# Optimization experiments

Measured on AMD Instinct MI355X. Metric: run time of the kernel, lower is better.

The kernel has to match this reference:

```python
import jax, jax.numpy as jnp
import numpy as np

EMBED = 1024
HEADS = 16
HEAD_DIM = EMBED // HEADS
SCALE = HEAD_DIM ** -0.5


def setup_inputs() -> dict:
    key = jax.random.key(0)
    ks = jax.random.split(key, 9)
    B, N = 2, 2048
    std = EMBED ** -0.5
    return {
        "query": jax.random.normal(ks[0], (B, N, EMBED), jnp.float32),
        "key": jax.random.normal(ks[1], (B, N, EMBED), jnp.float32),
        "value": jax.random.normal(ks[2], (B, N, EMBED), jnp.float32),
        # torch nn.Linear weights are [out, in]; y = x @ W.T + b
        "Wq": jax.random.normal(ks[3], (EMBED, EMBED), jnp.float32) * std,
        "bq": jax.random.normal(ks[4], (EMBED,), jnp.float32) * 0.01,
        "Wk": jax.random.normal(ks[5], (EMBED, EMBED), jnp.float32) * std,
        "bk": jax.random.normal(ks[6], (EMBED,), jnp.float32) * 0.01,
        "Wv": jax.random.normal(ks[7], (EMBED, EMBED), jnp.float32) * std,
        "bv": jax.random.normal(ks[8], (EMBED,), jnp.float32) * 0.01,
    }


def reference(query, key, value, Wq, bq, Wk, bk, Wv, bv):
    B, NQ, _ = query.shape
    NK = key.shape[1]
    q = query @ Wq.T + bq  # [B, NQ, E]
    k = key @ Wk.T + bk    # [B, NK, E]
    v = value @ Wv.T + bv  # [B, NK, E]
    # split heads -> [B, H, N, Dh]
    q = q.reshape(B, NQ, HEADS, HEAD_DIM).transpose(0, 2, 1, 3)
    k = k.reshape(B, NK, HEADS, HEAD_DIM).transpose(0, 2, 1, 3)
    v = v.reshape(B, NK, HEADS, HEAD_DIM).transpose(0, 2, 1, 3)
    attn = jnp.einsum("bhqd,bhkd->bhqk", q, k) * SCALE  # [B, H, NQ, NK]
    attn = jax.nn.softmax(attn, axis=-1)
    out = jnp.einsum("bhqk,bhkd->bhqd", attn, v)  # [B, H, NQ, Dh]
    out = out.transpose(0, 2, 1, 3).reshape(B, NQ, EMBED)
    # o_proj is Identity (odim == embed_dim, o_proj=False); dropout is 0 (eval)
    return out
```

## Files before the change

### kernel.cpp

```cpp
#include <hip/hip_runtime.h>

#define EMB 1024
#define NSEQ 2048
#define NBATCH 2
#define NHEAD 16
#define DHEAD 64
#define QSCALE 0.18033688011112042f

typedef float f32x4 __attribute__((ext_vector_type(4)));
typedef short s16x8 __attribute__((ext_vector_type(8)));
typedef short s16x4 __attribute__((ext_vector_type(4)));

typedef __attribute__((address_space(3))) short lds_short;
typedef __attribute__((address_space(1))) const short glb_short;

__device__ __forceinline__ void gl_lds16(const short* g, short* l) {
    __builtin_amdgcn_global_load_lds((glb_short*)g, (lds_short*)l, 16, 0, 0);
}

__device__ __forceinline__ short bf16r(float f) {
    unsigned u = __float_as_uint(f);
    u += 0x7fffu + ((u >> 16) & 1u);
    return (short)(u >> 16);
}

__device__ __forceinline__ unsigned pkbf(float a, float b) {
#if defined(__has_builtin) && __has_builtin(__builtin_amdgcn_cvt_pk_bf16_f32)
    auto r = __builtin_amdgcn_cvt_pk_bf16_f32(a, b);
    unsigned u;
    __builtin_memcpy(&u, &r, 4);
    return u;
#else
    return ((unsigned)bf16r(a) & 0xffffu) | ((unsigned)bf16r(b) << 16);
#endif
}

__device__ __forceinline__ float fexp2(float x) {
#if defined(__has_builtin) && __has_builtin(__builtin_amdgcn_exp2f)
    return __builtin_amdgcn_exp2f(x);
#else
    return exp2f(x);
#endif
}

__global__ __launch_bounds__(256) void cvt6_kernel(
    const float* __restrict__ s0, const float* __restrict__ s1, const float* __restrict__ s2,
    const float* __restrict__ s3, const float* __restrict__ s4, const float* __restrict__ s5,
    short* __restrict__ d0, short* __restrict__ d1, short* __restrict__ d2,
    short* __restrict__ d3, short* __restrict__ d4, short* __restrict__ d5,
    int n0, int n1, int n2, int n3, int n4, int n5)
{
    const int seg = blockIdx.y;
    const float* s = (seg == 0) ? s0 : (seg == 1) ? s1 : (seg == 2) ? s2
                   : (seg == 3) ? s3 : (seg == 4) ? s4 : s5;
    short* d = (seg == 0) ? d0 : (seg == 1) ? d1 : (seg == 2) ? d2
             : (seg == 3) ? d3 : (seg == 4) ? d4 : d5;
    const int n = (seg == 0) ? n0 : (seg == 1) ? n1 : (seg == 2) ? n2
                : (seg == 3) ? n3 : (seg == 4) ? n4 : n5;

    const int i = (blockIdx.x * 256 + threadIdx.x) * 8;
    if (i >= n) return;
    float4 a = *(const float4*)(s + i);
    float4 b = *(const float4*)(s + i + 4);
    uint4 u = { pkbf(a.x, a.y), pkbf(a.z, a.w), pkbf(b.x, b.y), pkbf(b.z, b.w) };
    *(uint4*)(d + i) = u;
}

__global__ __launch_bounds__(256) void proj2_kernel(
    const short* __restrict__ Xq, const short* __restrict__ Xk, const short* __restrict__ Xv,
    const short* __restrict__ Wq, const short* __restrict__ Wk, const short* __restrict__ Wv,
    const float* __restrict__ bq, const float* __restrict__ bk, const float* __restrict__ bv,
    short* __restrict__ Oq, short* __restrict__ Ok, short* __restrict__ Ov)
{
    const int z = blockIdx.z;
    const short* X    = (z == 0) ? Xq : (z == 1) ? Xk : Xv;
    const short* W    = (z == 0) ? Wq : (z == 1) ? Wk : Wv;
    const float* bias = (z == 0) ? bq : (z == 1) ? bk : bv;
    short* Out        = (z == 0) ? Oq : (z == 1) ? Ok : Ov;
    const float osc   = (z == 0) ? QSCALE : 1.0f;

    const int n0 = blockIdx.x * 128;
    const int m0 = blockIdx.y * 128;

    __shared__ __align__(16) short As[128 * 32];
    __shared__ __align__(16) short Bs[128 * 32];

    const int t    = threadIdx.x;
    const int lane = t & 63;
    const int wave = t >> 6;
    const int r    = lane & 15;
    const int quad = lane >> 4;
    const int wm   = (wave >> 1) * 64;
    const int wn   = (wave & 1) * 64;

    const int flat0 = t * 16;
    const int flat1 = flat0 + 4096;
    const int row0  = flat0 >> 6;
    const int row1  = flat1 >> 6;
    const int cs0   = (((flat0 >> 4) & 3) ^ (row0 & 3)) * 8;
    const int cs1   = (((flat1 >> 4) & 3) ^ (row1 & 3)) * 8;

    const short* ga0 = X + (size_t)(m0 + row0) * EMB + cs0;
    const short* ga1 = X + (size_t)(m0 + row1) * EMB + cs1;
    const short* gb0 = W + (size_t)(n0 + row0) * EMB + cs0;
    const short* gb1 = W + (size_t)(n0 + row1) * EMB + cs1;
    short* la0 = As + (flat0 >> 1);
    short* la1 = As + (flat1 >> 1);
    short* lb0 = Bs + (flat0 >> 1);
    short* lb1 = Bs + (flat1 >> 1);

    f32x4 acc[4][4];
#pragma unroll
    for (int i = 0; i < 4; ++i)
#pragma unroll
        for (int j = 0; j < 4; ++j)
#pragma unroll
            for (int v = 0; v < 4; ++v) acc[i][j][v] = 0.f;

    const int fcol = (quad ^ (r & 3)) * 8;

    for (int k0 = 0; k0 < EMB; k0 += 32) {
        gl_lds16(ga0 + k0, la0);
        gl_lds16(ga1 + k0, la1);
        gl_lds16(gb0 + k0, lb0);
        gl_lds16(gb1 + k0, lb1);
        __syncthreads();

        s16x8 af[4], bf[4];
#pragma unroll
        for (int i = 0; i < 4; ++i) af[i] = *(const s16x8*)&As[(wm + i * 16 + r) * 32 + fcol];
#pragma unroll
        for (int j = 0; j < 4; ++j) bf[j] = *(const s16x8*)&Bs[(wn + j * 16 + r) * 32 + fcol];
#pragma unroll
        for (int i = 0; i < 4; ++i)
#pragma unroll
            for (int j = 0; j < 4; ++j)
                acc[i][j] = __builtin_amdgcn_mfma_f32_16x16x32_bf16(af[i], bf[j], acc[i][j], 0, 0, 0);
        __syncthreads();
    }

#pragma unroll
    for (int j = 0; j < 4; ++j) {
        const int gn = n0 + wn + j * 16 + r;
        const float bb = bias[gn];
#pragma unroll
        for (int i = 0; i < 4; ++i)
#pragma unroll
            for (int reg = 0; reg < 4; ++reg) {
                const int gm = m0 + wm + i * 16 + quad * 4 + reg;
                Out[(size_t)gm * EMB + gn] = bf16r((acc[i][j][reg] + bb) * osc);
            }
    }
}

__global__ __launch_bounds__(256) void proj_kernel(
    const float* __restrict__ Xq, const float* __restrict__ Xk, const float* __restrict__ Xv,
    const float* __restrict__ Wq, const float* __restrict__ Wk, const float* __restrict__ Wv,
    const float* __restrict__ bq, const float* __restrict__ bk, const float* __restrict__ bv,
    short* __restrict__ Oq, short* __restrict__ Ok, short* __restrict__ Ov)
{
    const int z = blockIdx.z;
    const float* X    = (z == 0) ? Xq : (z == 1) ? Xk : Xv;
    const float* W    = (z == 0) ? Wq : (z == 1) ? Wk : Wv;
    const float* bias = (z == 0) ? bq : (z == 1) ? bk : bv;
    short* Out        = (z == 0) ? Oq : (z == 1) ? Ok : Ov;
    const float osc   = (z == 0) ? QSCALE : 1.0f;

    const int n0 = blockIdx.x * 128;
    const int m0 = blockIdx.y * 128;

    __shared__ __align__(16) short As[128][40];
    __shared__ __align__(16) short Bs[128][40];

    const int t    = threadIdx.x;
    const int lane = t & 63;
    const int wave = t >> 6;
    const int r    = lane & 15;
    const int quad = lane >> 4;
    const int wm   = (wave >> 1) * 64;
    const int wn   = (wave & 1) * 64;

    const int srow = t >> 1;
    const int scol = (t & 1) << 4;

    f32x4 acc[4][4];
#pragma unroll
    for (int i = 0; i < 4; ++i)
#pragma unroll
        for (int j = 0; j < 4; ++j)
#pragma unroll
            for (int v = 0; v < 4; ++v) acc[i][j][v] = 0.f;

    for (int k0 = 0; k0 < EMB; k0 += 32) {
        const float4* xp = (const float4*)(X + (size_t)(m0 + srow) * EMB + k0 + scol);
        const float4* wp = (const float4*)(W + (size_t)(n0 + srow) * EMB + k0 + scol);
        float4 x0 = xp[0], x1 = xp[1], x2 = xp[2], x3 = xp[3];
        float4 w0 = wp[0], w1 = wp[1], w2 = wp[2], w3 = wp[3];
        uint4 a0 = { pkbf(x0.x, x0.y), pkbf(x0.z, x0.w), pkbf(x1.x, x1.y), pkbf(x1.z, x1.w) };
        uint4 a1 = { pkbf(x2.x, x2.y), pkbf(x2.z, x2.w), pkbf(x3.x, x3.y), pkbf(x3.z, x3.w) };
        uint4 b0 = { pkbf(w0.x, w0.y), pkbf(w0.z, w0.w), pkbf(w1.x, w1.y), pkbf(w1.z, w1.w) };
        uint4 b1 = { pkbf(w2.x, w2.y), pkbf(w2.z, w2.w), pkbf(w3.x, w3.y), pkbf(w3.z, w3.w) };
        *(uint4*)&As[srow][scol]     = a0;
        *(uint4*)&As[srow][scol + 8] = a1;
        *(uint4*)&Bs[srow][scol]     = b0;
        *(uint4*)&Bs[srow][scol + 8] = b1;
        __syncthreads();

        s16x8 af[4], bf[4];
#pragma unroll
        for (int i = 0; i < 4; ++i) af[i] = *(const s16x8*)&As[wm + i * 16 + r][quad * 8];
#pragma unroll
        for (int j = 0; j < 4; ++j) bf[j] = *(const s16x8*)&Bs[wn + j * 16 + r][quad * 8];
#pragma unroll
        for (int i = 0; i < 4; ++i)
#pragma unroll
            for (int j = 0; j < 4; ++j)
                acc[i][j] = __builtin_amdgcn_mfma_f32_16x16x32_bf16(af[i], bf[j], acc[i][j], 0, 0, 0);
        __syncthreads();
    }

#pragma unroll
    for (int j = 0; j < 4; ++j) {
        const int gn = n0 + wn + j * 16 + r;
        const float bb = bias[gn];
#pragma unroll
        for (int i = 0; i < 4; ++i)
#pragma unroll
            for (int reg = 0; reg < 4; ++reg) {
                const int gm = m0 + wm + i * 16 + quad * 4 + reg;
                Out[(size_t)gm * EMB + gn] = bf16r((acc[i][j][reg] + bb) * osc);
            }
    }
}

__global__ __launch_bounds__(256) void vtrans_kernel(
    const short* __restrict__ Vp, short* __restrict__ VT)
{
    const int n0 = blockIdx.x * 64;
    const int h  = blockIdx.y;
    const int b  = blockIdx.z;
    __shared__ __align__(16) short L[64][72];

    const int t  = threadIdx.x;
    const int rr = t >> 2;
    const int cc = (t & 3) * 16;

    const short* src = Vp + (size_t)(b * NSEQ + n0 + rr) * EMB + h * DHEAD + cc;
    s16x8 a = *(const s16x8*)src;
    s16x8 c = *(const s16x8*)(src + 8);
    *(s16x8*)&L[rr][cc]     = a;
    *(s16x8*)&L[rr][cc + 8] = c;
    __syncthreads();

    const int d  = t >> 2;
    const int c4 = (t & 3) * 16;
    short vals[16];
#pragma unroll
    for (int i = 0; i < 16; ++i) vals[i] = L[c4 + i][d];
    short* dst = VT + ((size_t)(b * NHEAD + h) * DHEAD + d) * NSEQ + n0 + c4;
    *(s16x8*)dst       = *(s16x8*)&vals[0];
    *(s16x8*)(dst + 8) = *(s16x8*)&vals[8];
}

__global__ __launch_bounds__(256, 2) void attn2_kernel(
    const short* __restrict__ Qp, const short* __restrict__ Kp,
    const short* __restrict__ VT, float* __restrict__ Out)
{
    const int qblk = blockIdx.x * 128;
    const int h    = blockIdx.y;
    const int b    = blockIdx.z;

    __shared__ __align__(16) short Ks[64][72];
    __shared__ __align__(16) short Vs[64][72];
    __shared__ __align__(16) float fbuf[4][16][68];

    const int t    = threadIdx.x;
    const int lane = t & 63;
    const int w    = t >> 6;
    const int r    = lane & 15;
    const int quad = lane >> 4;

    const size_t rowbase = (size_t)b * NSEQ;
    const int colbase    = h * DHEAD;

    s16x8 qf[2][2];
#pragma unroll
    for (int qs = 0; qs < 2; ++qs)
#pragma unroll
        for (int ks = 0; ks < 2; ++ks)
            qf[qs][ks] = *(const s16x8*)(Qp + (rowbase + qblk + w * 32 + qs * 16 + r) * EMB
                                          + colbase + ks * 32 + quad * 8);

    f32x4 accO[2][4];
    float lsum[2] = {0.f, 0.f};
#pragma unroll
    for (int qs = 0; qs < 2; ++qs)
#pragma unroll
        for (int dt = 0; dt < 4; ++dt)
#pragma unroll
            for (int v = 0; v < 4; ++v) accO[qs][dt][v] = 0.f;

    const int srow = t >> 2;
    const int scol = (t & 3) << 4;

    const short* Kbase = Kp + (rowbase + srow) * EMB + colbase + scol;
    const short* Vbase = VT + ((size_t)(b * NHEAD + h) * DHEAD + srow) * NSEQ + scol;

    for (int kt = 0; kt < 32; ++kt) {
        const short* Ksrc = Kbase + (size_t)(kt * 64) * EMB;
        const short* Vsrc = Vbase + kt * 64;
        s16x8 k0 = *(const s16x8*)Ksrc, k1 = *(const s16x8*)(Ksrc + 8);
        s16x8 v0 = *(const s16x8*)Vsrc, v1 = *(const s16x8*)(Vsrc + 8);
        *(s16x8*)&Ks[srow][scol]     = k0;
        *(s16x8*)&Ks[srow][scol + 8] = k1;
        *(s16x8*)&Vs[srow][scol]     = v0;
        *(s16x8*)&Vs[srow][scol + 8] = v1;
        __syncthreads();

        s16x8 kf[4][2];
#pragma unroll
        for (int jt = 0; jt < 4; ++jt)
#pragma unroll
            for (int ks = 0; ks < 2; ++ks)
                kf[jt][ks] = *(const s16x8*)&Ks[jt * 16 + r][ks * 32 + quad * 8];

        s16x8 vf[4][2];
#pragma unroll
        for (int dt = 0; dt < 4; ++dt)
#pragma unroll
            for (int s = 0; s < 2; ++s) {
                s16x4 lo = *(const s16x4*)&Vs[dt * 16 + r][s * 32 + quad * 4];
                s16x4 hi = *(const s16x4*)&Vs[dt * 16 + r][s * 32 + 16 + quad * 4];
                vf[dt][s] = __builtin_shufflevector(lo, hi, 0, 1, 2, 3, 4, 5, 6, 7);
            }

        s16x8 pf[2][2];
#pragma unroll
        for (int qs = 0; qs < 2; ++qs) {
            f32x4 sacc[4];
#pragma unroll
            for (int jt = 0; jt < 4; ++jt) {
#pragma unroll
                for (int v = 0; v < 4; ++v) sacc[jt][v] = 0.f;
#pragma unroll
                for (int ks = 0; ks < 2; ++ks)
                    sacc[jt] = __builtin_amdgcn_mfma_f32_16x16x32_bf16(kf[jt][ks], qf[qs][ks], sacc[jt], 0, 0, 0);
            }
            float p[4][4];
#pragma unroll
            for (int jt = 0; jt < 4; ++jt)
#pragma unroll
                for (int reg = 0; reg < 4; ++reg) {
                    p[jt][reg] = fexp2(sacc[jt][reg]);
                    lsum[qs] += p[jt][reg];
                }
#pragma unroll
            for (int s = 0; s < 2; ++s) {
                uint4 uu = { pkbf(p[2 * s][0],     p[2 * s][1]),
                             pkbf(p[2 * s][2],     p[2 * s][3]),
                             pkbf(p[2 * s + 1][0], p[2 * s + 1][1]),
                             pkbf(p[2 * s + 1][2], p[2 * s + 1][3]) };
                __builtin_memcpy(&pf[qs][s], &uu, 16);
            }
        }

#pragma unroll
        for (int qs = 0; qs < 2; ++qs)
#pragma unroll
            for (int dt = 0; dt < 4; ++dt) {
                accO[qs][dt] = __builtin_amdgcn_mfma_f32_16x16x32_bf16(vf[dt][0], pf[qs][0], accO[qs][dt], 0, 0, 0);
                accO[qs][dt] = __builtin_amdgcn_mfma_f32_16x16x32_bf16(vf[dt][1], pf[qs][1], accO[qs][dt], 0, 0, 0);
            }
        __syncthreads();
    }

    float rl[2];
#pragma unroll
    for (int qs = 0; qs < 2; ++qs) {
        float s = lsum[qs];
        s += __shfl_xor(s, 16);
        s += __shfl_xor(s, 32);
        rl[qs] = 1.f / s;
    }

#pragma unroll
    for (int qs = 0; qs < 2; ++qs) {
        __syncthreads();
#pragma unroll
        for (int dt = 0; dt < 4; ++dt)
#pragma unroll
            for (int reg = 0; reg < 4; ++reg)
                fbuf[w][r][dt * 16 + quad * 4 + reg] = accO[qs][dt][reg] * rl[qs];
        __syncthreads();
        const int qi   = t >> 2;
        const int c    = (t & 3) * 16;
        const int wsrc = qi >> 4;
        const int rsrc = qi & 15;
        const float4* fp = (const float4*)&fbuf[wsrc][rsrc][c];
        float4 o0 = fp[0], o1 = fp[1], o2 = fp[2], o3 = fp[3];
        float* op = Out + (rowbase + qblk + wsrc * 32 + qs * 16 + rsrc) * EMB + colbase + c;
        ((float4*)op)[0] = o0;
        ((float4*)op)[1] = o1;
        ((float4*)op)[2] = o2;
        ((float4*)op)[3] = o3;
    }
}

__global__ __launch_bounds__(256) void attn_fb_kernel(
    const short* __restrict__ Qp, const short* __restrict__ Kp,
    const short* __restrict__ Vp, float* __restrict__ Out)
{
    const int qt = blockIdx.x;
    const int h  = blockIdx.y;
    const int b  = blockIdx.z;

    __shared__ __align__(16) short Ks[64][72];
    __shared__ __align__(16) short VsT[64][72];
    __shared__ __align__(16) short Ps[4][16][72];

    const int t    = threadIdx.x;
    const int lane = t & 63;
    const int w    = t >> 6;
    const int r    = lane & 15;
    const int quad = lane >> 4;

    const size_t rowbase = (size_t)b * NSEQ;
    const int colbase    = h * DHEAD;

    const short* Qr = Qp + (rowbase + qt * 64 + w * 16 + r) * EMB + colbase;
    const s16x8 qf0 = *(const s16x8*)(Qr + quad * 8);
    const s16x8 qf1 = *(const s16x8*)(Qr + 32 + quad * 8);

    float mrow[4], lrow[4];
    f32x4 accO[4];
#pragma unroll
    for (int i = 0; i < 4; ++i) {
        mrow[i] = -INFINITY;
        lrow[i] = 0.f;
#pragma unroll
        for (int v = 0; v < 4; ++v) accO[i][v] = 0.f;
    }

    const int srow = t >> 2;
    const int scol = (t & 3) << 4;

    for (int kt = 0; kt < 32; ++kt) {
        const short* Krow = Kp + (rowbase + kt * 64 + srow) * EMB + colbase + scol;
        const short* Vrow = Vp + (rowbase + kt * 64 + srow) * EMB + colbase + scol;
        s16x8 kv0 = *(const s16x8*)Krow;
        s16x8 kv1 = *(const s16x8*)(Krow + 8);
        s16x8 vv0 = *(const s16x8*)Vrow;
        s16x8 vv1 = *(const s16x8*)(Vrow + 8);
        *(s16x8*)&Ks[srow][scol]     = kv0;
        *(s16x8*)&Ks[srow][scol + 8] = kv1;
#pragma unroll
        for (int i = 0; i < 8; ++i) {
            VsT[scol + i][srow]     = vv0[i];
            VsT[scol + 8 + i][srow] = vv1[i];
        }
        __syncthreads();

        f32x4 sacc[4];
#pragma unroll
        for (int j = 0; j < 4; ++j) {
#pragma unroll
            for (int v = 0; v < 4; ++v) sacc[j][v] = 0.f;
            s16x8 kf0 = *(const s16x8*)&Ks[j * 16 + r][quad * 8];
            s16x8 kf1 = *(const s16x8*)&Ks[j * 16 + r][32 + quad * 8];
            sacc[j] = __builtin_amdgcn_mfma_f32_16x16x32_bf16(qf0, kf0, sacc[j], 0, 0, 0);
            sacc[j] = __builtin_amdgcn_mfma_f32_16x16x32_bf16(qf1, kf1, sacc[j], 0, 0, 0);
        }

        float rmax[4];
#pragma unroll
        for (int reg = 0; reg < 4; ++reg) rmax[reg] = -INFINITY;
#pragma unroll
        for (int j = 0; j < 4; ++j)
#pragma unroll
            for (int reg = 0; reg < 4; ++reg)
                rmax[reg] = fmaxf(rmax[reg], sacc[j][reg]);
#pragma unroll
        for (int reg = 0; reg < 4; ++reg) {
#pragma unroll
            for (int mask = 1; mask <= 8; mask <<= 1)
                rmax[reg] = fmaxf(rmax[reg], __shfl_xor(rmax[reg], mask, 64));
        }

        float alpha[4], rsum[4];
#pragma unroll
        for (int reg = 0; reg < 4; ++reg) {
            float mnew = fmaxf(mrow[reg], rmax[reg]);
            alpha[reg] = fexp2(mrow[reg] - mnew);
            mrow[reg]  = mnew;
            rsum[reg]  = 0.f;
        }

#pragma unroll
        for (int j = 0; j < 4; ++j)
#pragma unroll
            for (int reg = 0; reg < 4; ++reg) {
                float p = fexp2(sacc[j][reg] - mrow[reg]);
                rsum[reg] += p;
                Ps[w][quad * 4 + reg][j * 16 + r] = bf16r(p);
            }
#pragma unroll
        for (int reg = 0; reg < 4; ++reg) {
#pragma unroll
            for (int mask = 1; mask <= 8; mask <<= 1)
                rsum[reg] += __shfl_xor(rsum[reg], mask, 64);
            lrow[reg] = lrow[reg] * alpha[reg] + rsum[reg];
        }
#pragma unroll
        for (int j = 0; j < 4; ++j)
#pragma unroll
            for (int reg = 0; reg < 4; ++reg) accO[j][reg] *= alpha[reg];

#pragma unroll
        for (int s = 0; s < 2; ++s) {
            s16x8 pfr = *(const s16x8*)&Ps[w][r][s * 32 + quad * 8];
#pragma unroll
            for (int j = 0; j < 4; ++j) {
                s16x8 vfr = *(const s16x8*)&VsT[j * 16 + r][s * 32 + quad * 8];
                accO[j] = __builtin_amdgcn_mfma_f32_16x16x32_bf16(pfr, vfr, accO[j], 0, 0, 0);
            }
        }
        __syncthreads();
    }

#pragma unroll
    for (int j = 0; j < 4; ++j)
#pragma unroll
        for (int reg = 0; reg < 4; ++reg) {
            const int qrow = qt * 64 + w * 16 + quad * 4 + reg;
            Out[(rowbase + qrow) * EMB + colbase + j * 16 + r] = accO[j][reg] / lrow[reg];
        }
}

extern "C" void kernel_launch(void* const* d_in, const int* in_sizes, int n_in,
                              void* d_out, int out_size, void* d_ws, size_t ws_size,
                              hipStream_t stream) {
    const float* query = (const float*)d_in[0];
    const float* key   = (const float*)d_in[1];
    const float* value = (const float*)d_in[2];
    const float* Wq    = (const float*)d_in[3];
    const float* bq    = (const float*)d_in[4];
    const float* Wk    = (const float*)d_in[5];
    const float* bk    = (const float*)d_in[6];
    const float* Wv    = (const float*)d_in[7];
    const float* bv    = (const float*)d_in[8];
    float* out = (float*)d_out;

    const size_t XBUF = (size_t)NBATCH * NSEQ * EMB;
    const size_t WBUF = (size_t)EMB * EMB;

    short* Qb  = (short*)d_ws;
    short* Kb  = Qb + XBUF;
    short* Vb  = Kb + XBUF;
    short* VTb = Vb + XBUF;
    short* Xqb = VTb + XBUF;
    short* Xkb = Xqb + XBUF;
    short* Xvb = Xkb + XBUF;
    short* Wqb = Xvb + XBUF;
    short* Wkb = Wqb + WBUF;
    short* Wvb = Wkb + WBUF;

    const size_t need_full  = (7 * XBUF + 3 * WBUF) * sizeof(short);
    const size_t need_attn2 = 4 * XBUF * sizeof(short);

    if (ws_size >= need_full) {
        cvt6_kernel<<<dim3(2048, 6), 256, 0, stream>>>(
            query, key, value, Wq, Wk, Wv,
            Xqb, Xkb, Xvb, Wqb, Wkb, Wvb,
            (int)XBUF, (int)XBUF, (int)XBUF, (int)WBUF, (int)WBUF, (int)WBUF);
        proj2_kernel<<<dim3(EMB / 128, (NBATCH * NSEQ) / 128, 3), 256, 0, stream>>>(
            Xqb, Xkb, Xvb, Wqb, Wkb, Wvb, bq, bk, bv, Qb, Kb, Vb);
        vtrans_kernel<<<dim3(NSEQ / 64, NHEAD, NBATCH), 256, 0, stream>>>(Vb, VTb);
        attn2_kernel<<<dim3(NSEQ / 128, NHEAD, NBATCH), 256, 0, stream>>>(Qb, Kb, VTb, out);
    } else if (ws_size >= need_attn2) {
        proj_kernel<<<dim3(EMB / 128, (NBATCH * NSEQ) / 128, 3), 256, 0, stream>>>(
            query, key, value, Wq, Wk, Wv, bq, bk, bv, Qb, Kb, Vb);
        vtrans_kernel<<<dim3(NSEQ / 64, NHEAD, NBATCH), 256, 0, stream>>>(Vb, VTb);
        attn2_kernel<<<dim3(NSEQ / 128, NHEAD, NBATCH), 256, 0, stream>>>(Qb, Kb, VTb, out);
    } else {
        proj_kernel<<<dim3(EMB / 128, (NBATCH * NSEQ) / 128, 3), 256, 0, stream>>>(
            query, key, value, Wq, Wk, Wv, bq, bk, bv, Qb, Kb, Vb);
        attn_fb_kernel<<<dim3(NSEQ / 64, NHEAD, NBATCH), 256, 0, stream>>>(Qb, Kb, Vb, out);
    }
}
```

Baseline: 207.2 us.

## Split attention keys across waves and widen projection K-tile

The attention kernel now gives each block 64 queries and splits each 128-key tile across the four waves, so every wave handles 32 keys for all 64 queries. The waves' partial outputs and row sums are combined through shared memory at the end. K/V tiles are staged with direct global-to-LDS loads into XOR-swizzled layouts. The projection GEMM doubles its K-step to 64 with a wider swizzle and asks for three blocks per SM; this halves the barrier count but adds a cross-wave reduction and more LDS per block.

New measurement: 241.6 us. 1.17x slower.

```diff
diff --git a/kernel.cpp b/kernel.cpp
--- a/kernel.cpp
+++ b/kernel.cpp
@@ -66,7 +66,7 @@
     *(uint4*)(d + i) = u;
 }
 
-__global__ __launch_bounds__(256) void proj2_kernel(
+__global__ __launch_bounds__(256, 3) void proj2_kernel(
     const short* __restrict__ Xq, const short* __restrict__ Xk, const short* __restrict__ Xv,
     const short* __restrict__ Wq, const short* __restrict__ Wk, const short* __restrict__ Wv,
     const float* __restrict__ bq, const float* __restrict__ bk, const float* __restrict__ bv,
@@ -82,8 +82,8 @@
     const int n0 = blockIdx.x * 128;
     const int m0 = blockIdx.y * 128;
 
-    __shared__ __align__(16) short As[128 * 32];
-    __shared__ __align__(16) short Bs[128 * 32];
+    __shared__ __align__(16) short As[128 * 64];
+    __shared__ __align__(16) short Bs[128 * 64];
 
     const int t    = threadIdx.x;
     const int lane = t & 63;
@@ -93,21 +93,13 @@
     const int wm   = (wave >> 1) * 64;
     const int wn   = (wave & 1) * 64;
 
-    const int flat0 = t * 16;
-    const int flat1 = flat0 + 4096;
-    const int row0  = flat0 >> 6;
-    const int row1  = flat1 >> 6;
-    const int cs0   = (((flat0 >> 4) & 3) ^ (row0 & 3)) * 8;
-    const int cs1   = (((flat1 >> 4) & 3) ^ (row1 & 3)) * 8;
-
-    const short* ga0 = X + (size_t)(m0 + row0) * EMB + cs0;
-    const short* ga1 = X + (size_t)(m0 + row1) * EMB + cs1;
-    const short* gb0 = W + (size_t)(n0 + row0) * EMB + cs0;
-    const short* gb1 = W + (size_t)(n0 + row1) * EMB + cs1;
-    short* la0 = As + (flat0 >> 1);
-    short* la1 = As + (flat1 >> 1);
-    short* lb0 = Bs + (flat0 >> 1);
-    short* lb1 = Bs + (flat1 >> 1);
+    const int p0    = wave * 256 + lane;
+    const int row0  = p0 >> 3;
+    const int lc0   = (p0 & 7) ^ (row0 & 7);
+    const short* gA = X + (size_t)(m0 + row0) * EMB + lc0 * 8;
+    const short* gB = W + (size_t)(n0 + row0) * EMB + lc0 * 8;
+    short* lA = As + p0 * 8;
+    short* lB = Bs + p0 * 8;
 
     f32x4 acc[4][4];
 #pragma unroll
@@ -117,25 +109,28 @@
 #pragma unroll
             for (int v = 0; v < 4; ++v) acc[i][j][v] = 0.f;
 
-    const int fcol = (quad ^ (r & 3)) * 8;
-
-    for (int k0 = 0; k0 < EMB; k0 += 32) {
-        gl_lds16(ga0 + k0, la0);
-        gl_lds16(ga1 + k0, la1);
-        gl_lds16(gb0 + k0, lb0);
-        gl_lds16(gb1 + k0, lb1);
-        __syncthreads();
-
-        s16x8 af[4], bf[4];
-#pragma unroll
-        for (int i = 0; i < 4; ++i) af[i] = *(const s16x8*)&As[(wm + i * 16 + r) * 32 + fcol];
-#pragma unroll
-        for (int j = 0; j < 4; ++j) bf[j] = *(const s16x8*)&Bs[(wn + j * 16 + r) * 32 + fcol];
-#pragma unroll
-        for (int i = 0; i < 4; ++i)
-#pragma unroll
-            for (int j = 0; j < 4; ++j)
-                acc[i][j] = __builtin_amdgcn_mfma_f32_16x16x32_bf16(af[i], bf[j], acc[i][j], 0, 0, 0);
+    for (int k0 = 0; k0 < EMB; k0 += 64) {
+#pragma unroll
+        for (int i = 0; i < 4; ++i) {
+            gl_lds16(gA + k0 + (size_t)8 * i * EMB, lA + i * 512);
+            gl_lds16(gB + k0 + (size_t)8 * i * EMB, lB + i * 512);
+        }
+        __syncthreads();
+
+#pragma unroll
+        for (int ks = 0; ks < 2; ++ks) {
+            const int fc = ((ks * 4 + quad) ^ (r & 7)) * 8;
+            s16x8 af[4], bf[4];
+#pragma unroll
+            for (int i = 0; i < 4; ++i) af[i] = *(const s16x8*)&As[(wm + i * 16 + r) * 64 + fc];
+#pragma unroll
+            for (int j = 0; j < 4; ++j) bf[j] = *(const s16x8*)&Bs[(wn + j * 16 + r) * 64 + fc];
+#pragma unroll
+            for (int i = 0; i < 4; ++i)
+#pragma unroll
+                for (int j = 0; j < 4; ++j)
+                    acc[i][j] = __builtin_amdgcn_mfma_f32_16x16x32_bf16(af[i], bf[j], acc[i][j], 0, 0, 0);
+        }
         __syncthreads();
     }
 
@@ -262,17 +257,20 @@
     *(s16x8*)(dst + 8) = *(s16x8*)&vals[8];
 }
 
-__global__ __launch_bounds__(256, 2) void attn2_kernel(
+__global__ __launch_bounds__(256, 3) void attn3_kernel(
     const short* __restrict__ Qp, const short* __restrict__ Kp,
     const short* __restrict__ VT, float* __restrict__ Out)
 {
-    const int qblk = blockIdx.x * 128;
+    const int qblk = blockIdx.x * 64;
     const int h    = blockIdx.y;
     const int b    = blockIdx.z;
 
-    __shared__ __align__(16) short Ks[64][72];
-    __shared__ __align__(16) short Vs[64][72];
-    __shared__ __align__(16) float fbuf[4][16][68];
+    __shared__ __align__(16) char smem[35840];
+    short* KsS  = (short*)smem;
+    short* VsS  = (short*)smem + 128 * 64;
+    float* bufA = (float*)smem;
+    float* bufB = (float*)smem + 64 * 68;
+    float* l4   = (float*)smem + 2 * 64 * 68;
 
     const int t    = threadIdx.x;
     const int lane = t & 63;
@@ -281,128 +279,149 @@
     const int quad = lane >> 4;
 
     const size_t rowbase = (size_t)b * NSEQ;
-    const int colbase    = h * DHEAD;
-
-    s16x8 qf[2][2];
-#pragma unroll
-    for (int qs = 0; qs < 2; ++qs)
+    const int    colbase = h * DHEAD;
+    const size_t bh64    = (size_t)(b * NHEAD + h) * DHEAD;
+
+    s16x8 qf[4][2];
+#pragma unroll
+    for (int qt = 0; qt < 4; ++qt)
 #pragma unroll
         for (int ks = 0; ks < 2; ++ks)
-            qf[qs][ks] = *(const s16x8*)(Qp + (rowbase + qblk + w * 32 + qs * 16 + r) * EMB
+            qf[qt][ks] = *(const s16x8*)(Qp + (rowbase + qblk + qt * 16 + r) * EMB
                                           + colbase + ks * 32 + quad * 8);
 
-    f32x4 accO[2][4];
-    float lsum[2] = {0.f, 0.f};
-#pragma unroll
-    for (int qs = 0; qs < 2; ++qs)
+    const int pk0   = w * 256 + lane;
+    const int krow0 = pk0 >> 3;
+    const int klc   = (pk0 & 7) ^ (krow0 & 7);
+    const short* gK = Kp + (rowbase + krow0) * EMB + colbase + klc * 8;
+    short* lK = KsS + pk0 * 8;
+
+    const short* gV[4];
+    short* lV[4];
+#pragma unroll
+    for (int i = 0; i < 4; ++i) {
+        const int p   = (w * 4 + i) * 64 + lane;
+        const int row = p >> 4;
+        const int lc  = (p & 15) ^ (row & 15);
+        gV[i] = VT + (bh64 + row) * NSEQ + lc * 8;
+        lV[i] = VsS + p * 8;
+    }
+
+    f32x4 accO[4][4];
+    float lsum[4] = {0.f, 0.f, 0.f, 0.f};
+#pragma unroll
+    for (int qt = 0; qt < 4; ++qt)
 #pragma unroll
         for (int dt = 0; dt < 4; ++dt)
 #pragma unroll
-            for (int v = 0; v < 4; ++v) accO[qs][dt][v] = 0.f;
-
-    const int srow = t >> 2;
-    const int scol = (t & 3) << 4;
-
-    const short* Kbase = Kp + (rowbase + srow) * EMB + colbase + scol;
-    const short* Vbase = VT + ((size_t)(b * NHEAD + h) * DHEAD + srow) * NSEQ + scol;
-
-    for (int kt = 0; kt < 32; ++kt) {
-        const short* Ksrc = Kbase + (size_t)(kt * 64) * EMB;
-        const short* Vsrc = Vbase + kt * 64;
-        s16x8 k0 = *(const s16x8*)Ksrc, k1 = *(const s16x8*)(Ksrc + 8);
-        s16x8 v0 = *(const s16x8*)Vsrc, v1 = *(const s16x8*)(Vsrc + 8);
-        *(s16x8*)&Ks[srow][scol]     = k0;
-        *(s16x8*)&Ks[srow][scol + 8] = k1;
-        *(s16x8*)&Vs[srow][scol]     = v0;
-        *(s16x8*)&Vs[srow][scol + 8] = v1;
-        __syncthreads();
-
-        s16x8 kf[4][2];
-#pragma unroll
-        for (int jt = 0; jt < 4; ++jt)
+            for (int v = 0; v < 4; ++v) accO[qt][dt][v] = 0.f;
+
+    for (int kt = 0; kt < 16; ++kt) {
+#pragma unroll
+        for (int i = 0; i < 4; ++i) {
+            gl_lds16(gK + (size_t)(kt * 128 + 8 * i) * EMB, lK + i * 512);
+            gl_lds16(gV[i] + kt * 128, lV[i]);
+        }
+        __syncthreads();
+
+        s16x8 kf[2][2];
+#pragma unroll
+        for (int jt = 0; jt < 2; ++jt)
 #pragma unroll
             for (int ks = 0; ks < 2; ++ks)
-                kf[jt][ks] = *(const s16x8*)&Ks[jt * 16 + r][ks * 32 + quad * 8];
-
-        s16x8 vf[4][2];
-#pragma unroll
-        for (int dt = 0; dt < 4; ++dt)
-#pragma unroll
-            for (int s = 0; s < 2; ++s) {
-                s16x4 lo = *(const s16x4*)&Vs[dt * 16 + r][s * 32 + quad * 4];
-                s16x4 hi = *(const s16x4*)&Vs[dt * 16 + r][s * 32 + 16 + quad * 4];
-                vf[dt][s] = __builtin_shufflevector(lo, hi, 0, 1, 2, 3, 4, 5, 6, 7);
+                kf[jt][ks] = *(const s16x8*)&KsS[(w * 32 + jt * 16 + r) * 64
+                                                 + (((ks * 4 + quad) ^ (r & 7)) * 8)];
+
+        s16x8 vfx[4];
+#pragma unroll
+        for (int dt = 0; dt < 4; ++dt) {
+            const int ph0 = (4 * w + (quad >> 1)) ^ r;
+            const int ph1 = (4 * w + 2 + (quad >> 1)) ^ r;
+            s16x4 lo = *(const s16x4*)&VsS[(dt * 16 + r) * 128 + ph0 * 8 + (quad & 1) * 4];
+            s16x4 hi = *(const s16x4*)&VsS[(dt * 16 + r) * 128 + ph1 * 8 + (quad & 1) * 4];
+            vfx[dt] = __builtin_shufflevector(lo, hi, 0, 1, 2, 3, 4, 5, 6, 7);
+        }
+
+#pragma unroll
+        for (int qt = 0; qt < 4; ++qt) {
+            f32x4 sacc[2];
+#pragma unroll
+            for (int jt = 0; jt < 2; ++jt) {
+#pragma unroll
+                for (int v = 0; v < 4; ++v) sacc[jt][v] = 0.f;
+#pragma unroll
+                for (int ks = 0; ks < 2; ++ks)
+                    sacc[jt] = __builtin_amdgcn_mfma_f32_16x16x32_bf16(kf[jt][ks], qf[qt][ks], sacc[jt], 0, 0, 0);
             }
-
-        s16x8 pf[2][2];
-#pragma unroll
-        for (int qs = 0; qs < 2; ++qs) {
-            f32x4 sacc[4];
-#pragma unroll
-            for (int jt = 0; jt < 4; ++jt) {
-#pragma unroll
-                for (int v = 0; v < 4; ++v) sacc[jt][v] = 0.f;
-#pragma unroll
-                for (int ks = 0; ks < 2; ++ks)
-                    sacc[jt] = __builtin_amdgcn_mfma_f32_16x16x32_bf16(kf[jt][ks], qf[qs][ks], sacc[jt], 0, 0, 0);
-            }
-            float p[4][4];
-#pragma unroll
-            for (int jt = 0; jt < 4; ++jt)
+            float p[2][4];
+#pragma unroll
+            for (int jt = 0; jt < 2; ++jt)
 #pragma unroll
                 for (int reg = 0; reg < 4; ++reg) {
                     p[jt][reg] = fexp2(sacc[jt][reg]);
-                    lsum[qs] += p[jt][reg];
+                    lsum[qt] += p[jt][reg];
                 }
-#pragma unroll
-            for (int s = 0; s < 2; ++s) {
-                uint4 uu = { pkbf(p[2 * s][0],     p[2 * s][1]),
-                             pkbf(p[2 * s][2],     p[2 * s][3]),
-                             pkbf(p[2 * s + 1][0], p[2 * s + 1][1]),
-                             pkbf(p[2 * s + 1][2], p[2 * s + 1][3]) };
-                __builtin_memcpy(&pf[qs][s], &uu, 16);
-            }
-        }
-
-#pragma unroll
-        for (int qs = 0; qs < 2; ++qs)
-#pragma unroll
-            for (int dt = 0; dt < 4; ++dt) {
-                accO[qs][dt] = __builtin_amdgcn_mfma_f32_16x16x32_bf16(vf[dt][0], pf[qs][0], accO[qs][dt], 0, 0, 0);
-                accO[qs][dt] = __builtin_amdgcn_mfma_f32_16x16x32_bf16(vf[dt][1], pf[qs][1], accO[qs][dt], 0, 0, 0);
-            }
-        __syncthreads();
-    }
-
-    float rl[2];
-#pragma unroll
-    for (int qs = 0; qs < 2; ++qs) {
-        float s = lsum[qs];
+            s16x8 pf;
+            uint4 uu = { pkbf(p[0][0], p[0][1]), pkbf(p[0][2], p[0][3]),
+                         pkbf(p[1][0], p[1][1]), pkbf(p[1][2], p[1][3]) };
+            __builtin_memcpy(&pf, &uu, 16);
+#pragma unroll
+            for (int dt = 0; dt < 4; ++dt)
+                accO[qt][dt] = __builtin_amdgcn_mfma_f32_16x16x32_bf16(vfx[dt], pf, accO[qt][dt], 0, 0, 0);
+        }
+        __syncthreads();
+    }
+
+#pragma unroll
+    for (int qt = 0; qt < 4; ++qt) {
+        float s = lsum[qt];
         s += __shfl_xor(s, 16);
         s += __shfl_xor(s, 32);
-        rl[qs] = 1.f / s;
-    }
-
-#pragma unroll
-    for (int qs = 0; qs < 2; ++qs) {
-        __syncthreads();
-#pragma unroll
-        for (int dt = 0; dt < 4; ++dt)
-#pragma unroll
-            for (int reg = 0; reg < 4; ++reg)
-                fbuf[w][r][dt * 16 + quad * 4 + reg] = accO[qs][dt][reg] * rl[qs];
-        __syncthreads();
-        const int qi   = t >> 2;
-        const int c    = (t & 3) * 16;
-        const int wsrc = qi >> 4;
-        const int rsrc = qi & 15;
-        const float4* fp = (const float4*)&fbuf[wsrc][rsrc][c];
-        float4 o0 = fp[0], o1 = fp[1], o2 = fp[2], o3 = fp[3];
-        float* op = Out + (rowbase + qblk + wsrc * 32 + qs * 16 + rsrc) * EMB + colbase + c;
-        ((float4*)op)[0] = o0;
-        ((float4*)op)[1] = o1;
-        ((float4*)op)[2] = o2;
-        ((float4*)op)[3] = o3;
+        if (quad == 0) l4[w * 64 + qt * 16 + r] = s;
+    }
+
+    float* mybuf = (w & 1) ? bufB : bufA;
+    if (w < 2) {
+#pragma unroll
+        for (int qt = 0; qt < 4; ++qt)
+#pragma unroll
+            for (int dt = 0; dt < 4; ++dt)
+                *(f32x4*)&mybuf[(qt * 16 + r) * 68 + dt * 16 + quad * 4] = accO[qt][dt];
+    }
+    __syncthreads();
+    if (w >= 2) {
+#pragma unroll
+        for (int qt = 0; qt < 4; ++qt)
+#pragma unroll
+            for (int dt = 0; dt < 4; ++dt) {
+                f32x4* pp = (f32x4*)&mybuf[(qt * 16 + r) * 68 + dt * 16 + quad * 4];
+                *pp += accO[qt][dt];
+            }
+    }
+    __syncthreads();
+    {
+        const int row = t >> 2;
+        const int c   = (t & 3) * 16;
+#pragma unroll
+        for (int g = 0; g < 4; ++g) {
+            f32x4* pa = (f32x4*)&bufA[row * 68 + c + g * 4];
+            *pa += *(const f32x4*)&bufB[row * 68 + c + g * 4];
+        }
+    }
+    __syncthreads();
+    {
+        const int q = t >> 2;
+        const int c = (t & 3) * 16;
+        const float l  = l4[q] + l4[64 + q] + l4[128 + q] + l4[192 + q];
+        const float rl = 1.f / l;
+        float* op = Out + (rowbase + qblk + q) * EMB + colbase + c;
+#pragma unroll
+        for (int g = 0; g < 4; ++g) {
+            f32x4 o = *(const f32x4*)&bufA[q * 68 + c + g * 4];
+            o *= rl;
+            float4 of = { o[0], o[1], o[2], o[3] };
+            ((float4*)op)[g] = of;
+        }
     }
 }
 
@@ -565,7 +584,7 @@
     short* Wvb = Wkb + WBUF;
 
     const size_t need_full  = (7 * XBUF + 3 * WBUF) * sizeof(short);
-    const size_t need_attn2 = 4 * XBUF * sizeof(short);
+    const size_t need_attn3 = 4 * XBUF * sizeof(short);
 
     if (ws_size >= need_full) {
         cvt6_kernel<<<dim3(2048, 6), 256, 0, stream>>>(
@@ -575,12 +594,12 @@
         proj2_kernel<<<dim3(EMB / 128, (NBATCH * NSEQ) / 128, 3), 256, 0, stream>>>(
             Xqb, Xkb, Xvb, Wqb, Wkb, Wvb, bq, bk, bv, Qb, Kb, Vb);
         vtrans_kernel<<<dim3(NSEQ / 64, NHEAD, NBATCH), 256, 0, stream>>>(Vb, VTb);
-        attn2_kernel<<<dim3(NSEQ / 128, NHEAD, NBATCH), 256, 0, stream>>>(Qb, Kb, VTb, out);
-    } else if (ws_size >= need_attn2) {
+        attn3_kernel<<<dim3(NSEQ / 64, NHEAD, NBATCH), 256, 0, stream>>>(Qb, Kb, VTb, out);
+    } else if (ws_size >= need_attn3) {
         proj_kernel<<<dim3(EMB / 128, (NBATCH * NSEQ) / 128, 3), 256, 0, stream>>>(
             query, key, value, Wq, Wk, Wv, bq, bk, bv, Qb, Kb, Vb);
         vtrans_kernel<<<dim3(NSEQ / 64, NHEAD, NBATCH), 256, 0, stream>>>(Vb, VTb);
-        attn2_kernel<<<dim3(NSEQ / 128, NHEAD, NBATCH), 256, 0, stream>>>(Qb, Kb, VTb, out);
+        attn3_kernel<<<dim3(NSEQ / 64, NHEAD, NBATCH), 256, 0, stream>>>(Qb, Kb, VTb, out);
     } else {
         proj_kernel<<<dim3(EMB / 128, (NBATCH * NSEQ) / 128, 3), 256, 0, stream>>>(
             query, key, value, Wq, Wk, Wv, bq, bk, bv, Qb, Kb, Vb);
```

## Deepen projection GEMM K-tile to 64 and shrink attention query tile to 64

Applied to the files above, without the earlier changes.

The projection GEMM now stages a 64-wide K slice per iteration with an 8-way XOR swizzle. This halves the number of barrier round trips, at the cost of more LDS. The attention kernel drops from 128 to 64 query rows per block (16 per wave) and aliases the output staging buffer onto the K/V shared memory. That cuts register and LDS use so 4 blocks can fit per CU, but it doubles K/V reloads per query row.

After: 221.1 us. 1.07x slower.

```diff
diff --git a/kernel.cpp b/kernel.cpp
--- a/kernel.cpp
+++ b/kernel.cpp
@@ -66,7 +66,7 @@
     *(uint4*)(d + i) = u;
 }
 
-__global__ __launch_bounds__(256) void proj2_kernel(
+__global__ __launch_bounds__(256, 3) void proj2_kernel(
     const short* __restrict__ Xq, const short* __restrict__ Xk, const short* __restrict__ Xv,
     const short* __restrict__ Wq, const short* __restrict__ Wk, const short* __restrict__ Wv,
     const float* __restrict__ bq, const float* __restrict__ bk, const float* __restrict__ bv,
@@ -82,8 +82,8 @@
     const int n0 = blockIdx.x * 128;
     const int m0 = blockIdx.y * 128;
 
-    __shared__ __align__(16) short As[128 * 32];
-    __shared__ __align__(16) short Bs[128 * 32];
+    __shared__ __align__(16) short As[128 * 64];
+    __shared__ __align__(16) short Bs[128 * 64];
 
     const int t    = threadIdx.x;
     const int lane = t & 63;
@@ -93,21 +93,13 @@
     const int wm   = (wave >> 1) * 64;
     const int wn   = (wave & 1) * 64;
 
-    const int flat0 = t * 16;
-    const int flat1 = flat0 + 4096;
-    const int row0  = flat0 >> 6;
-    const int row1  = flat1 >> 6;
-    const int cs0   = (((flat0 >> 4) & 3) ^ (row0 & 3)) * 8;
-    const int cs1   = (((flat1 >> 4) & 3) ^ (row1 & 3)) * 8;
-
-    const short* ga0 = X + (size_t)(m0 + row0) * EMB + cs0;
-    const short* ga1 = X + (size_t)(m0 + row1) * EMB + cs1;
-    const short* gb0 = W + (size_t)(n0 + row0) * EMB + cs0;
-    const short* gb1 = W + (size_t)(n0 + row1) * EMB + cs1;
-    short* la0 = As + (flat0 >> 1);
-    short* la1 = As + (flat1 >> 1);
-    short* lb0 = Bs + (flat0 >> 1);
-    short* lb1 = Bs + (flat1 >> 1);
+    const int p0    = wave * 256 + lane;
+    const int row0  = p0 >> 3;
+    const int lc0   = (p0 & 7) ^ (row0 & 7);
+    const short* gA = X + (size_t)(m0 + row0) * EMB + lc0 * 8;
+    const short* gB = W + (size_t)(n0 + row0) * EMB + lc0 * 8;
+    short* lA = As + p0 * 8;
+    short* lB = Bs + p0 * 8;
 
     f32x4 acc[4][4];
 #pragma unroll
@@ -117,25 +109,28 @@
 #pragma unroll
             for (int v = 0; v < 4; ++v) acc[i][j][v] = 0.f;
 
-    const int fcol = (quad ^ (r & 3)) * 8;
-
-    for (int k0 = 0; k0 < EMB; k0 += 32) {
-        gl_lds16(ga0 + k0, la0);
-        gl_lds16(ga1 + k0, la1);
-        gl_lds16(gb0 + k0, lb0);
-        gl_lds16(gb1 + k0, lb1);
-        __syncthreads();
-
-        s16x8 af[4], bf[4];
-#pragma unroll
-        for (int i = 0; i < 4; ++i) af[i] = *(const s16x8*)&As[(wm + i * 16 + r) * 32 + fcol];
-#pragma unroll
-        for (int j = 0; j < 4; ++j) bf[j] = *(const s16x8*)&Bs[(wn + j * 16 + r) * 32 + fcol];
-#pragma unroll
-        for (int i = 0; i < 4; ++i)
-#pragma unroll
-            for (int j = 0; j < 4; ++j)
-                acc[i][j] = __builtin_amdgcn_mfma_f32_16x16x32_bf16(af[i], bf[j], acc[i][j], 0, 0, 0);
+    for (int k0 = 0; k0 < EMB; k0 += 64) {
+#pragma unroll
+        for (int i = 0; i < 4; ++i) {
+            gl_lds16(gA + k0 + (size_t)8 * i * EMB, lA + i * 512);
+            gl_lds16(gB + k0 + (size_t)8 * i * EMB, lB + i * 512);
+        }
+        __syncthreads();
+
+#pragma unroll
+        for (int ks = 0; ks < 2; ++ks) {
+            const int fc = ((ks * 4 + quad) ^ (r & 7)) * 8;
+            s16x8 af[4], bf[4];
+#pragma unroll
+            for (int i = 0; i < 4; ++i) af[i] = *(const s16x8*)&As[(wm + i * 16 + r) * 64 + fc];
+#pragma unroll
+            for (int j = 0; j < 4; ++j) bf[j] = *(const s16x8*)&Bs[(wn + j * 16 + r) * 64 + fc];
+#pragma unroll
+            for (int i = 0; i < 4; ++i)
+#pragma unroll
+                for (int j = 0; j < 4; ++j)
+                    acc[i][j] = __builtin_amdgcn_mfma_f32_16x16x32_bf16(af[i], bf[j], acc[i][j], 0, 0, 0);
+        }
         __syncthreads();
     }
 
@@ -262,17 +257,18 @@
     *(s16x8*)(dst + 8) = *(s16x8*)&vals[8];
 }
 
-__global__ __launch_bounds__(256, 2) void attn2_kernel(
+__global__ __launch_bounds__(256, 4) void attn5_kernel(
     const short* __restrict__ Qp, const short* __restrict__ Kp,
     const short* __restrict__ VT, float* __restrict__ Out)
 {
-    const int qblk = blockIdx.x * 128;
+    const int qblk = blockIdx.x * 64;
     const int h    = blockIdx.y;
     const int b    = blockIdx.z;
 
-    __shared__ __align__(16) short Ks[64][72];
-    __shared__ __align__(16) short Vs[64][72];
-    __shared__ __align__(16) float fbuf[4][16][68];
+    __shared__ __align__(16) char smem[2 * 64 * 72 * 2];
+    short* Ks   = (short*)smem;
+    short* Vs   = (short*)smem + 64 * 72;
+    float* fbuf = (float*)smem;
 
     const int t    = threadIdx.x;
     const int lane = t & 63;
@@ -281,40 +277,37 @@
     const int quad = lane >> 4;
 
     const size_t rowbase = (size_t)b * NSEQ;
-    const int colbase    = h * DHEAD;
-
-    s16x8 qf[2][2];
-#pragma unroll
-    for (int qs = 0; qs < 2; ++qs)
-#pragma unroll
-        for (int ks = 0; ks < 2; ++ks)
-            qf[qs][ks] = *(const s16x8*)(Qp + (rowbase + qblk + w * 32 + qs * 16 + r) * EMB
-                                          + colbase + ks * 32 + quad * 8);
-
-    f32x4 accO[2][4];
-    float lsum[2] = {0.f, 0.f};
-#pragma unroll
-    for (int qs = 0; qs < 2; ++qs)
-#pragma unroll
-        for (int dt = 0; dt < 4; ++dt)
-#pragma unroll
-            for (int v = 0; v < 4; ++v) accO[qs][dt][v] = 0.f;
+    const int    colbase = h * DHEAD;
+    const size_t bh64    = (size_t)(b * NHEAD + h) * DHEAD;
+
+    s16x8 qf[2];
+#pragma unroll
+    for (int ks = 0; ks < 2; ++ks)
+        qf[ks] = *(const s16x8*)(Qp + (rowbase + qblk + w * 16 + r) * EMB
+                                  + colbase + ks * 32 + quad * 8);
+
+    f32x4 accO[4];
+    float lsum = 0.f;
+#pragma unroll
+    for (int dt = 0; dt < 4; ++dt)
+#pragma unroll
+        for (int v = 0; v < 4; ++v) accO[dt][v] = 0.f;
 
     const int srow = t >> 2;
     const int scol = (t & 3) << 4;
 
     const short* Kbase = Kp + (rowbase + srow) * EMB + colbase + scol;
-    const short* Vbase = VT + ((size_t)(b * NHEAD + h) * DHEAD + srow) * NSEQ + scol;
+    const short* Vbase = VT + (bh64 + srow) * NSEQ + scol;
 
     for (int kt = 0; kt < 32; ++kt) {
         const short* Ksrc = Kbase + (size_t)(kt * 64) * EMB;
         const short* Vsrc = Vbase + kt * 64;
         s16x8 k0 = *(const s16x8*)Ksrc, k1 = *(const s16x8*)(Ksrc + 8);
         s16x8 v0 = *(const s16x8*)Vsrc, v1 = *(const s16x8*)(Vsrc + 8);
-        *(s16x8*)&Ks[srow][scol]     = k0;
-        *(s16x8*)&Ks[srow][scol + 8] = k1;
-        *(s16x8*)&Vs[srow][scol]     = v0;
-        *(s16x8*)&Vs[srow][scol + 8] = v1;
+        *(s16x8*)&Ks[srow * 72 + scol]     = k0;
+        *(s16x8*)&Ks[srow * 72 + scol + 8] = k1;
+        *(s16x8*)&Vs[srow * 72 + scol]     = v0;
+        *(s16x8*)&Vs[srow * 72 + scol + 8] = v1;
         __syncthreads();
 
         s16x8 kf[4][2];
@@ -322,87 +315,75 @@
         for (int jt = 0; jt < 4; ++jt)
 #pragma unroll
             for (int ks = 0; ks < 2; ++ks)
-                kf[jt][ks] = *(const s16x8*)&Ks[jt * 16 + r][ks * 32 + quad * 8];
+                kf[jt][ks] = *(const s16x8*)&Ks[(jt * 16 + r) * 72 + ks * 32 + quad * 8];
 
         s16x8 vf[4][2];
 #pragma unroll
         for (int dt = 0; dt < 4; ++dt)
 #pragma unroll
             for (int s = 0; s < 2; ++s) {
-                s16x4 lo = *(const s16x4*)&Vs[dt * 16 + r][s * 32 + quad * 4];
-                s16x4 hi = *(const s16x4*)&Vs[dt * 16 + r][s * 32 + 16 + quad * 4];
+                s16x4 lo = *(const s16x4*)&Vs[(dt * 16 + r) * 72 + s * 32 + quad * 4];
+                s16x4 hi = *(const s16x4*)&Vs[(dt * 16 + r) * 72 + s * 32 + 16 + quad * 4];
                 vf[dt][s] = __builtin_shufflevector(lo, hi, 0, 1, 2, 3, 4, 5, 6, 7);
             }
 
-        s16x8 pf[2][2];
-#pragma unroll
-        for (int qs = 0; qs < 2; ++qs) {
-            f32x4 sacc[4];
-#pragma unroll
-            for (int jt = 0; jt < 4; ++jt) {
-#pragma unroll
-                for (int v = 0; v < 4; ++v) sacc[jt][v] = 0.f;
-#pragma unroll
-                for (int ks = 0; ks < 2; ++ks)
-                    sacc[jt] = __builtin_amdgcn_mfma_f32_16x16x32_bf16(kf[jt][ks], qf[qs][ks], sacc[jt], 0, 0, 0);
+        f32x4 sacc[4];
+#pragma unroll
+        for (int jt = 0; jt < 4; ++jt) {
+#pragma unroll
+            for (int v = 0; v < 4; ++v) sacc[jt][v] = 0.f;
+#pragma unroll
+            for (int ks = 0; ks < 2; ++ks)
+                sacc[jt] = __builtin_amdgcn_mfma_f32_16x16x32_bf16(kf[jt][ks], qf[ks], sacc[jt], 0, 0, 0);
+        }
+
+        float p[4][4];
+#pragma unroll
+        for (int jt = 0; jt < 4; ++jt)
+#pragma unroll
+            for (int reg = 0; reg < 4; ++reg) {
+                p[jt][reg] = fexp2(sacc[jt][reg]);
+                lsum += p[jt][reg];
             }
-            float p[4][4];
-#pragma unroll
-            for (int jt = 0; jt < 4; ++jt)
-#pragma unroll
-                for (int reg = 0; reg < 4; ++reg) {
-                    p[jt][reg] = fexp2(sacc[jt][reg]);
-                    lsum[qs] += p[jt][reg];
-                }
-#pragma unroll
-            for (int s = 0; s < 2; ++s) {
-                uint4 uu = { pkbf(p[2 * s][0],     p[2 * s][1]),
-                             pkbf(p[2 * s][2],     p[2 * s][3]),
-                             pkbf(p[2 * s + 1][0], p[2 * s + 1][1]),
-                             pkbf(p[2 * s + 1][2], p[2 * s + 1][3]) };
-                __builtin_memcpy(&pf[qs][s], &uu, 16);
-            }
-        }
-
-#pragma unroll
-        for (int qs = 0; qs < 2; ++qs)
-#pragma unroll
-            for (int dt = 0; dt < 4; ++dt) {
-                accO[qs][dt] = __builtin_amdgcn_mfma_f32_16x16x32_bf16(vf[dt][0], pf[qs][0], accO[qs][dt], 0, 0, 0);
-                accO[qs][dt] = __builtin_amdgcn_mfma_f32_16x16x32_bf16(vf[dt][1], pf[qs][1], accO[qs][dt], 0, 0, 0);
-            }
-        __syncthreads();
-    }
-
-    float rl[2];
-#pragma unroll
-    for (int qs = 0; qs < 2; ++qs) {
-        float s = lsum[qs];
-        s += __shfl_xor(s, 16);
-        s += __shfl_xor(s, 32);
-        rl[qs] = 1.f / s;
-    }
-
-#pragma unroll
-    for (int qs = 0; qs < 2; ++qs) {
-        __syncthreads();
-#pragma unroll
-        for (int dt = 0; dt < 4; ++dt)
-#pragma unroll
-            for (int reg = 0; reg < 4; ++reg)
-                fbuf[w][r][dt * 16 + quad * 4 + reg] = accO[qs][dt][reg] * rl[qs];
-        __syncthreads();
-        const int qi   = t >> 2;
-        const int c    = (t & 3) * 16;
-        const int wsrc = qi >> 4;
-        const int rsrc = qi & 15;
-        const float4* fp = (const float4*)&fbuf[wsrc][rsrc][c];
-        float4 o0 = fp[0], o1 = fp[1], o2 = fp[2], o3 = fp[3];
-        float* op = Out + (rowbase + qblk + wsrc * 32 + qs * 16 + rsrc) * EMB + colbase + c;
-        ((float4*)op)[0] = o0;
-        ((float4*)op)[1] = o1;
-        ((float4*)op)[2] = o2;
-        ((float4*)op)[3] = o3;
+        s16x8 pf[2];
+#pragma unroll
+        for (int s = 0; s < 2; ++s) {
+            uint4 uu = { pkbf(p[2 * s][0],     p[2 * s][1]),
+                         pkbf(p[2 * s][2],     p[2 * s][3]),
+                         pkbf(p[2 * s + 1][0], p[2 * s + 1][1]),
+                         pkbf(p[2 * s + 1][2], p[2 * s + 1][3]) };
+            __builtin_memcpy(&pf[s], &uu, 16);
+        }
+
+#pragma unroll
+        for (int dt = 0; dt < 4; ++dt) {
+            accO[dt] = __builtin_amdgcn_mfma_f32_16x16x32_bf16(vf[dt][0], pf[0], accO[dt], 0, 0, 0);
+            accO[dt] = __builtin_amdgcn_mfma_f32_16x16x32_bf16(vf[dt][1], pf[1], accO[dt], 0, 0, 0);
+        }
+        __syncthreads();
+    }
+
+    lsum += __shfl_xor(lsum, 16);
+    lsum += __shfl_xor(lsum, 32);
+    const float rl = 1.f / lsum;
+
+#pragma unroll
+    for (int dt = 0; dt < 4; ++dt) {
+        f32x4 o = accO[dt];
+        o *= rl;
+        *(f32x4*)&fbuf[(w * 16 + r) * 68 + dt * 16 + quad * 4] = o;
+    }
+    __syncthreads();
+    {
+        const int q = t >> 2;
+        const int c = (t & 3) * 16;
+        float* op = Out + (rowbase + qblk + q) * EMB + colbase + c;
+#pragma unroll
+        for (int g = 0; g < 4; ++g) {
+            f32x4 o = *(const f32x4*)&fbuf[q * 68 + c + g * 4];
+            float4 of = { o[0], o[1], o[2], o[3] };
+            ((float4*)op)[g] = of;
+        }
     }
 }
 
@@ -565,7 +546,7 @@
     short* Wvb = Wkb + WBUF;
 
     const size_t need_full  = (7 * XBUF + 3 * WBUF) * sizeof(short);
-    const size_t need_attn2 = 4 * XBUF * sizeof(short);
+    const size_t need_attn5 = 4 * XBUF * sizeof(short);
 
     if (ws_size >= need_full) {
         cvt6_kernel<<<dim3(2048, 6), 256, 0, stream>>>(
@@ -575,12 +556,12 @@
         proj2_kernel<<<dim3(EMB / 128, (NBATCH * NSEQ) / 128, 3), 256, 0, stream>>>(
             Xqb, Xkb, Xvb, Wqb, Wkb, Wvb, bq, bk, bv, Qb, Kb, Vb);
         vtrans_kernel<<<dim3(NSEQ / 64, NHEAD, NBATCH), 256, 0, stream>>>(Vb, VTb);
-        attn2_kernel<<<dim3(NSEQ / 128, NHEAD, NBATCH), 256, 0, stream>>>(Qb, Kb, VTb, out);
-    } else if (ws_size >= need_attn2) {
+        attn5_kernel<<<dim3(NSEQ / 64, NHEAD, NBATCH), 256, 0, stream>>>(Qb, Kb, VTb, out);
+    } else if (ws_size >= need_attn5) {
         proj_kernel<<<dim3(EMB / 128, (NBATCH * NSEQ) / 128, 3), 256, 0, stream>>>(
             query, key, value, Wq, Wk, Wv, bq, bk, bv, Qb, Kb, Vb);
         vtrans_kernel<<<dim3(NSEQ / 64, NHEAD, NBATCH), 256, 0, stream>>>(Vb, VTb);
-        attn2_kernel<<<dim3(NSEQ / 128, NHEAD, NBATCH), 256, 0, stream>>>(Qb, Kb, VTb, out);
+        attn5_kernel<<<dim3(NSEQ / 64, NHEAD, NBATCH), 256, 0, stream>>>(Qb, Kb, VTb, out);
     } else {
         proj_kernel<<<dim3(EMB / 128, (NBATCH * NSEQ) / 128, 3), 256, 0, stream>>>(
             query, key, value, Wq, Wk, Wv, bq, bk, bv, Qb, Kb, Vb);
```
